# Kernel tuning notes

Measured on AMD Instinct MI355X. Metric: run time of the kernel, lower is better.

The kernel has to match this reference:

```python
import jax, jax.numpy as jnp
import numpy as np
from jax import lax

EPSILON = 0.01
CLAMP_MIN = 0.8
CLAMP_MAX = 1.2


def setup_inputs() -> dict:
    key = jax.random.key(0)
    k1, k2, k3, k4 = jax.random.split(key, 4)
    B, T, D = 8, 4096, 1024
    write_signal = jax.random.normal(k1, (B, T, D), dtype=jnp.float32)
    pad_mask = jax.random.randint(k2, (B, T), 0, 2) == 1
    update_mask = jax.random.randint(k3, (B, T), 0, 2) == 1
    # trust_proj weight (dim -> 1, no bias); scaled small for a varied tanh regime
    w = jax.random.normal(k4, (D,), dtype=jnp.float32) * 0.02
    return {"write_signal": write_signal, "pad_mask": pad_mask,
            "update_mask": update_mask, "w": w}


def reference(write_signal, pad_mask, update_mask, w):
    # write_signal: (B, T, D); pad_mask/update_mask: (B, T) bool; w: (D,)
    B, T, D = write_signal.shape
    dtype = write_signal.dtype
    # gate_t = (~pad) * update, per the torch code's multiplied float masks
    gate = ((~pad_mask) & update_mask).astype(dtype)  # (B, T)

    def step(mem, inp):
        x_t, g_t = inp                      # x_t: (B, D), g_t: (B,)
        g = g_t[:, None]
        mem = (1.0 - EPSILON * g) * mem + EPSILON * x_t * g
        bias = 1.0 + jnp.tanh(mem @ w)      # (B,)
        return mem, bias

    xs = (jnp.swapaxes(write_signal, 0, 1), gate.T)  # time-major
    mem0 = jnp.zeros((B, D), dtype=dtype)
    memory, biases = lax.scan(step, mem0, xs)        # biases: (T, B)
    bias_stack = biases.T                            # (B, T)
    bias_stack = jnp.where(pad_mask, jnp.asarray(1.0, dtype), bias_stack)
    bias_stack = jnp.clip(bias_stack, CLAMP_MIN, CLAMP_MAX)
    return bias_stack, memory
```

## Files before the change

### kernel.cpp

```cpp
#include <hip/hip_runtime.h>

#define EPS 0.01f
#define B_ 8
#define T_ 4096
#define D_ 1024

__global__ __launch_bounds__(1024) void gate_alpha_kernel(
    const int* __restrict__ pad, const int* __restrict__ upd,
    float* __restrict__ alpha) {
    const int b = blockIdx.x;
    const int tid = threadIdx.x;
    const int base = b * T_;

    const int4 pv = reinterpret_cast<const int4*>(pad + base)[tid];
    const int4 uv = reinterpret_cast<const int4*>(upd + base)[tid];
    int g[4];
    g[0] = (pv.x == 0 && uv.x != 0) ? 1 : 0;
    g[1] = (pv.y == 0 && uv.y != 0) ? 1 : 0;
    g[2] = (pv.z == 0 && uv.z != 0) ? 1 : 0;
    g[3] = (pv.w == 0 && uv.w != 0) ? 1 : 0;
    const int cnt = g[0] + g[1] + g[2] + g[3];

    __shared__ int s[1024];
    s[tid] = cnt;
    __syncthreads();
    for (int off = 1; off < 1024; off <<= 1) {
        int v = s[tid];
        int add = (tid >= off) ? s[tid - off] : 0;
        __syncthreads();
        s[tid] = v + add;
        __syncthreads();
    }
    const int total = s[1023];
    int c = s[tid] - cnt;

    const float L = -0.014499569695115089f;
    float4 av;
    float* ap = &av.x;
    #pragma unroll
    for (int i = 0; i < 4; ++i) {
        c += g[i];
        ap[i] = g[i] ? EPS * exp2f((float)(total - c) * L) : 0.f;
    }
    reinterpret_cast<float4*>(alpha + base)[tid] = av;
}

#define TCHUNK 64
#define NBLK_T (T_ / TCHUNK)
__global__ __launch_bounds__(1024) void main_pass_kernel(
    const float* __restrict__ x, const float* __restrict__ w,
    const float* __restrict__ alpha, float* __restrict__ y,
    float* __restrict__ mem_part) {
    const int b = blockIdx.y;
    const int tbase = blockIdx.x * TCHUNK;
    const int tid = threadIdx.x;
    const int wave = tid >> 6;
    const int lane = tid & 63;

    float4 wv[4];
    #pragma unroll
    for (int k = 0; k < 4; ++k)
        wv[k] = *reinterpret_cast<const float4*>(w + k * 256 + lane * 4);

    float4 acc[4];
    #pragma unroll
    for (int k = 0; k < 4; ++k) acc[k] = make_float4(0.f, 0.f, 0.f, 0.f);

    #pragma unroll
    for (int r = wave; r < TCHUNK; r += 16) {
        const int t = tbase + r;
        const float al = alpha[b * T_ + t];
        if (al == 0.f) continue;
        const float* row = x + ((size_t)b * T_ + t) * D_;
        float dot = 0.f;
        #pragma unroll
        for (int k = 0; k < 4; ++k) {
            float4 v = *reinterpret_cast<const float4*>(row + k * 256 + lane * 4);
            dot += v.x * wv[k].x + v.y * wv[k].y + v.z * wv[k].z + v.w * wv[k].w;
            acc[k].x += al * v.x;
            acc[k].y += al * v.y;
            acc[k].z += al * v.z;
            acc[k].w += al * v.w;
        }
        #pragma unroll
        for (int off = 32; off >= 1; off >>= 1)
            dot += __shfl_xor(dot, off);
        if (lane == 0) y[b * T_ + t] = dot;
    }

    __shared__ float part[16][D_];
    #pragma unroll
    for (int k = 0; k < 4; ++k)
        *reinterpret_cast<float4*>(&part[wave][k * 256 + lane * 4]) = acc[k];
    __syncthreads();
    float sum = 0.f;
    #pragma unroll
    for (int w2 = 0; w2 < 16; ++w2) sum += part[w2][tid];
    mem_part[((size_t)b * NBLK_T + blockIdx.x) * D_ + tid] = sum;
}

__global__ __launch_bounds__(1024) void finalize_kernel(
    const float* __restrict__ y, const int* __restrict__ pad,
    const int* __restrict__ upd, const float* __restrict__ mem_part,
    float* __restrict__ bias, float* __restrict__ mem) {
    if (blockIdx.x >= B_) {
        const int b = blockIdx.x - B_;
        const int d = threadIdx.x;
        float sum = 0.f;
        #pragma unroll
        for (int i = 0; i < NBLK_T; ++i)
            sum += mem_part[((size_t)b * NBLK_T + i) * D_ + d];
        mem[b * D_ + d] = sum;
        return;
    }

    const int b = blockIdx.x;
    const int tid = threadIdx.x;
    const int base = b * T_;

    const int4 pv = reinterpret_cast<const int4*>(pad + base)[tid];
    const int4 uv = reinterpret_cast<const int4*>(upd + base)[tid];
    const float4 yv = reinterpret_cast<const float4*>(y + base)[tid];
    int g[4];
    g[0] = (pv.x == 0 && uv.x != 0) ? 1 : 0;
    g[1] = (pv.y == 0 && uv.y != 0) ? 1 : 0;
    g[2] = (pv.z == 0 && uv.z != 0) ? 1 : 0;
    g[3] = (pv.w == 0 && uv.w != 0) ? 1 : 0;
    const float yl[4] = {yv.x, yv.y, yv.z, yv.w};

    float av[4], uvv[4];
    float a_c = 1.f, u_c = 0.f;
    #pragma unroll
    for (int i = 0; i < 4; ++i) {
        float a = g[i] ? (1.f - EPS) : 1.f;
        float u = g[i] ? EPS * yl[i] : 0.f;
        av[i] = a; uvv[i] = u;
        u_c = a * u_c + u;
        a_c = a * a_c;
    }

    __shared__ float As[1024], Us[1024];
    As[tid] = a_c; Us[tid] = u_c;
    __syncthreads();
    for (int off = 1; off < 1024; off <<= 1) {
        float A2 = As[tid], U2 = Us[tid];
        float A1 = (tid >= off) ? As[tid - off] : 1.f;
        float U1 = (tid >= off) ? Us[tid - off] : 0.f;
        __syncthreads();
        As[tid] = A1 * A2;
        Us[tid] = A2 * U1 + U2;
        __syncthreads();
    }
    float s = (tid > 0) ? Us[tid - 1] : 0.f;

    const int pl[4] = {pv.x, pv.y, pv.z, pv.w};
    float4 bv;
    float* bp = &bv.x;
    #pragma unroll
    for (int i = 0; i < 4; ++i) {
        s = av[i] * s + uvv[i];
        float bval;
        if (pl[i] != 0) {
            bval = 1.f;
        } else {
            bval = 1.f + tanhf(s);
            bval = fminf(fmaxf(bval, 0.8f), 1.2f);
        }
        bp[i] = bval;
    }
    reinterpret_cast<float4*>(bias + base)[tid] = bv;
}

extern "C" void kernel_launch(void* const* d_in, const int* in_sizes, int n_in,
                              void* d_out, int out_size, void* d_ws, size_t ws_size,
                              hipStream_t stream) {
    const float* x  = (const float*)d_in[0];
    const int* pad  = (const int*)d_in[1];
    const int* upd  = (const int*)d_in[2];
    const float* w  = (const float*)d_in[3];

    float* out  = (float*)d_out;
    float* bias = out;
    float* mem  = out + B_ * T_;

    float* alpha    = (float*)d_ws;
    float* y        = alpha + B_ * T_;
    float* mem_part = y + B_ * T_;

    gate_alpha_kernel<<<B_, 1024, 0, stream>>>(pad, upd, alpha);
    dim3 grid2(NBLK_T, B_);
    main_pass_kernel<<<grid2, 1024, 0, stream>>>(x, w, alpha, y, mem_part);
    finalize_kernel<<<2 * B_, 1024, 0, stream>>>(y, pad, upd, mem_part, bias, mem);
}
```

Before: 199.5 us.

## Fuse gate/alpha scan into main pass and double time chunk size

Drops the separate gate_alpha kernel. Each main-pass block now redundantly recomputes the full per-batch gate prefix scan in shared memory and keeps only the alpha values for its own time chunk. TCHUNK also goes from 64 to 128, which halves the number of blocks and partial-memory rows that finalize has to reduce. The aim is to save a kernel launch and the alpha round-trip through global memory, at the cost of a redundant 10-step block scan in every block and less parallelism.

```diff
diff --git a/kernel.cpp b/kernel.cpp
--- a/kernel.cpp
+++ b/kernel.cpp
@@ -5,57 +5,51 @@
 #define T_ 4096
 #define D_ 1024
 
-__global__ __launch_bounds__(1024) void gate_alpha_kernel(
-    const int* __restrict__ pad, const int* __restrict__ upd,
-    float* __restrict__ alpha) {
-    const int b = blockIdx.x;
-    const int tid = threadIdx.x;
-    const int base = b * T_;
-
-    const int4 pv = reinterpret_cast<const int4*>(pad + base)[tid];
-    const int4 uv = reinterpret_cast<const int4*>(upd + base)[tid];
-    int g[4];
-    g[0] = (pv.x == 0 && uv.x != 0) ? 1 : 0;
-    g[1] = (pv.y == 0 && uv.y != 0) ? 1 : 0;
-    g[2] = (pv.z == 0 && uv.z != 0) ? 1 : 0;
-    g[3] = (pv.w == 0 && uv.w != 0) ? 1 : 0;
-    const int cnt = g[0] + g[1] + g[2] + g[3];
-
-    __shared__ int s[1024];
-    s[tid] = cnt;
-    __syncthreads();
-    for (int off = 1; off < 1024; off <<= 1) {
-        int v = s[tid];
-        int add = (tid >= off) ? s[tid - off] : 0;
-        __syncthreads();
-        s[tid] = v + add;
-        __syncthreads();
-    }
-    const int total = s[1023];
-    int c = s[tid] - cnt;
-
-    const float L = -0.014499569695115089f;
-    float4 av;
-    float* ap = &av.x;
-    #pragma unroll
-    for (int i = 0; i < 4; ++i) {
-        c += g[i];
-        ap[i] = g[i] ? EPS * exp2f((float)(total - c) * L) : 0.f;
-    }
-    reinterpret_cast<float4*>(alpha + base)[tid] = av;
-}
-
-#define TCHUNK 64
+#define TCHUNK 128
 #define NBLK_T (T_ / TCHUNK)
 __global__ __launch_bounds__(1024) void main_pass_kernel(
     const float* __restrict__ x, const float* __restrict__ w,
-    const float* __restrict__ alpha, float* __restrict__ y,
-    float* __restrict__ mem_part) {
+    const int* __restrict__ pad, const int* __restrict__ upd,
+    float* __restrict__ y, float* __restrict__ mem_part) {
     const int b = blockIdx.y;
     const int tbase = blockIdx.x * TCHUNK;
     const int tid = threadIdx.x;
     const int wave = tid >> 6;
     const int lane = tid & 63;
+    const int base = b * T_;
+
+    __shared__ int s_scan[1024];
+    __shared__ float alpha_s[TCHUNK];
+    {
+        const int4 pv = reinterpret_cast<const int4*>(pad + base)[tid];
+        const int4 uv = reinterpret_cast<const int4*>(upd + base)[tid];
+        int g[4];
+        g[0] = (pv.x == 0 && uv.x != 0) ? 1 : 0;
+        g[1] = (pv.y == 0 && uv.y != 0) ? 1 : 0;
+        g[2] = (pv.z == 0 && uv.z != 0) ? 1 : 0;
+        g[3] = (pv.w == 0 && uv.w != 0) ? 1 : 0;
+        const int cnt = g[0] + g[1] + g[2] + g[3];
+        s_scan[tid] = cnt;
+        __syncthreads();
+        for (int off = 1; off < 1024; off <<= 1) {
+            int v = s_scan[tid];
+            int add = (tid >= off) ? s_scan[tid - off] : 0;
+            __syncthreads();
+            s_scan[tid] = v + add;
+            __syncthreads();
+        }
+        const int total = s_scan[1023];
+        int c = s_scan[tid] - cnt;
+        const float L = -0.014499569695115089f;
+        #pragma unroll
+        for (int i = 0; i < 4; ++i) {
+            const int t = 4 * tid + i;
+            c += g[i];
+            if (t >= tbase && t < tbase + TCHUNK)
+                alpha_s[t - tbase] = g[i] ? EPS * exp2f((float)(total - c) * L) : 0.f;
+        }
+    }
+    __syncthreads();
 
     float4 wv[4];
     #pragma unroll
@@ -66,26 +60,27 @@
     #pragma unroll
     for (int k = 0; k < 4; ++k) acc[k] = make_float4(0.f, 0.f, 0.f, 0.f);
 
-    #pragma unroll
     for (int r = wave; r < TCHUNK; r += 16) {
+        const float al = alpha_s[r];
         const int t = tbase + r;
-        const float al = alpha[b * T_ + t];
-        if (al == 0.f) continue;
-        const float* row = x + ((size_t)b * T_ + t) * D_;
+        const float* row = x + ((size_t)base + t) * D_ - (size_t)base * D_ + (size_t)b * T_ * D_;
+        const float* rowp = x + ((size_t)b * T_ + t) * D_;
         float dot = 0.f;
-        #pragma unroll
-        for (int k = 0; k < 4; ++k) {
-            float4 v = *reinterpret_cast<const float4*>(row + k * 256 + lane * 4);
-            dot += v.x * wv[k].x + v.y * wv[k].y + v.z * wv[k].z + v.w * wv[k].w;
-            acc[k].x += al * v.x;
-            acc[k].y += al * v.y;
-            acc[k].z += al * v.z;
-            acc[k].w += al * v.w;
+        if (al != 0.f) {
+            #pragma unroll
+            for (int k = 0; k < 4; ++k) {
+                float4 v = *reinterpret_cast<const float4*>(rowp + k * 256 + lane * 4);
+                dot += v.x * wv[k].x + v.y * wv[k].y + v.z * wv[k].z + v.w * wv[k].w;
+                acc[k].x += al * v.x;
+                acc[k].y += al * v.y;
+                acc[k].z += al * v.z;
+                acc[k].w += al * v.w;
+            }
+            #pragma unroll
+            for (int off = 32; off >= 1; off >>= 1)
+                dot += __shfl_xor(dot, off);
+            if (lane == 0) y[b * T_ + t] = dot;
         }
-        #pragma unroll
-        for (int off = 32; off >= 1; off >>= 1)
-            dot += __shfl_xor(dot, off);
-        if (lane == 0) y[b * T_ + t] = dot;
     }
 
     __shared__ float part[16][D_];
@@ -183,12 +178,10 @@
     float* bias = out;
     float* mem  = out + B_ * T_;
 
-    float* alpha    = (float*)d_ws;
-    float* y        = alpha + B_ * T_;
+    float* y        = (float*)d_ws;
     float* mem_part = y + B_ * T_;
 
-    gate_alpha_kernel<<<B_, 1024, 0, stream>>>(pad, upd, alpha);
-    dim3 grid2(NBLK_T, B_);
-    main_pass_kernel<<<grid2, 1024, 0, stream>>>(x, w, alpha, y, mem_part);
+    dim3 gridA(NBLK_T, B_);
+    main_pass_kernel<<<gridA, 1024, 0, stream>>>(x, w, pad, upd, y, mem_part);
     finalize_kernel<<<2 * B_, 1024, 0, stream>>>(y, pad, upd, mem_part, bias, mem);
 }
```

New measurement: 184.3 us. -7.6%, faster.
